# Kernel tuning notes

Hardware: AMD Instinct MI355X
Metric: run time of the kernel (lower is better)

Reference implementation:

```python
import jax, jax.numpy as jnp
import numpy as np

NOT_EPSILON = 1.0
B, Q, K, T = 2, 512, 512, 256  # batch, num queries, num keys, dims


def swishmax(x, axis):
    # x * exp(x - max) / (sum(|x * exp(x - max)|) + 1)
    xexp = x * jnp.exp(x - jnp.max(x, axis=axis, keepdims=True))
    return xexp / (jnp.sum(jnp.abs(xexp), axis=axis, keepdims=True) + NOT_EPSILON)


def setup_inputs() -> dict:
    key = jax.random.key(0)
    ks = jax.random.split(key, 8)
    s = 1.0 / np.sqrt(T)
    return {
        "query_tokens": jax.random.normal(ks[0], (B, Q, T), jnp.float32),
        "key_tokens": jax.random.normal(ks[1], (B, K, T), jnp.float32),
        "value_tokens": jax.random.normal(ks[2], (B, K, T), jnp.float32),
        "Wk": jax.random.normal(ks[3], (T, T), jnp.float32) * s,
        "Wq": jax.random.normal(ks[4], (T, T), jnp.float32) * s,
        "Wva": jax.random.normal(ks[5], (T, T), jnp.float32) * s,
        "Wal": jax.random.normal(ks[6], (T, T), jnp.float32) * s,
        "Wvo": jax.random.normal(ks[7], (T, T), jnp.float32) * s,
    }


def reference(query_tokens, key_tokens, value_tokens, Wk, Wq, Wva, Wal, Wvo):
    # torch nn.Linear: y = x @ W.T (no biases)
    k = jnp.einsum('bkt,ut->bku', key_tokens, Wk)      # [B,K,T]
    q = jnp.einsum('bqt,ut->bqu', query_tokens, Wq)    # [B,Q,T]
    # elementwise outer product over token pairs: [B,K,Q,T]
    raw = k[:, :, None, :] * q[:, None, :, :]
    logits = jnp.einsum('bkqt,ut->bkqu', raw, Wal)     # [B,K,Q,T]
    scale = swishmax(logits, axis=-2)                  # normalize over Q
    v = jnp.einsum('bkt,ut->bku', value_tokens, Wva)   # [B,K,T]
    values_scaled = v[:, :, None, :] * scale           # [B,K,Q,T]
    value_sum = values_scaled.sum(axis=-3)             # sum over K -> [B,Q,T]
    return jnp.einsum('bqt,ut->bqu', value_sum, Wvo)   # [B,Q,T]
```

## Files before the change

### kernel.cpp

```cpp
#include <hip/hip_runtime.h>
#include <cstdint>


typedef short bf16x8 __attribute__((ext_vector_type(8)));
typedef float f32x4  __attribute__((ext_vector_type(4)));

__device__ inline float bf2f(short s) {
  return __uint_as_float(((unsigned)(unsigned short)s) << 16);
}
__device__ inline unsigned packrn(float lo, float hi) {
  return __builtin_amdgcn_perm(__float_as_uint(hi) + 0x8000u,
                               __float_as_uint(lo) + 0x8000u, 0x07060302u);
}

#define FMA16()                                                                 \
  c[0][0] += a.x*w.x; c[0][1] += a.x*w.y; c[0][2] += a.x*w.z; c[0][3] += a.x*w.w; \
  c[1][0] += a.y*w.x; c[1][1] += a.y*w.y; c[1][2] += a.y*w.z; c[1][3] += a.y*w.w; \
  c[2][0] += a.z*w.x; c[2][1] += a.z*w.y; c[2][2] += a.z*w.z; c[2][3] += a.z*w.w; \
  c[3][0] += a.w*w.x; c[3][1] += a.w*w.y; c[3][2] += a.w*w.z; c[3][3] += a.w*w.w;

#define GEMM_BODY(X, WT)                                                        \
  __shared__ __align__(16) float As[16][68];                                    \
  __shared__ __align__(16) float Ws[16][64];                                    \
  const int tid = threadIdx.x;                                                  \
  const int tx4 = (tid & 15) * 4;                                               \
  const int ty4 = (tid >> 4) * 4;                                               \
  const int m0 = blockIdx.x * 64, u0 = blockIdx.y * 64;                         \
  const int lmi = tid >> 2, lc4 = (tid & 3) * 4;                                \
  const int lr  = tid >> 4, lu4 = (tid & 15) * 4;                               \
  float c[4][4] = {};                                                           \
  _Pragma("unroll 1")                                                           \
  for (int t0 = 0; t0 < 256; t0 += 16) {                                        \
    const float4 xa = *(const float4*)&(X)[(size_t)(m0 + lmi) * 256 + t0 + lc4];\
    const float4 wb = *(const float4*)&(WT)[(size_t)(t0 + lr) * 256 + u0 + lu4];\
    __syncthreads();                                                            \
    As[lc4 + 0][lmi] = xa.x; As[lc4 + 1][lmi] = xa.y;                           \
    As[lc4 + 2][lmi] = xa.z; As[lc4 + 3][lmi] = xa.w;                           \
    *(float4*)&Ws[lr][lu4] = wb;                                                \
    __syncthreads();                                                            \
    _Pragma("unroll")                                                           \
    for (int t = 0; t < 16; ++t) {                                              \
      const float4 a = *(const float4*)&As[t][ty4];                             \
      const float4 w = *(const float4*)&Ws[t][tx4];                             \
      FMA16();                                                                  \
    }                                                                           \
  }

__global__ __launch_bounds__(256) void prep(
    const float* __restrict__ Wk, const float* __restrict__ Wq,
    const float* __restrict__ Wva, const float* __restrict__ Wvo,
    const float* __restrict__ Wal, float* __restrict__ WT,
    short* __restrict__ WalF)
{
  const int r = blockIdx.x;
  const int m = blockIdx.y;
  const int t = threadIdx.x;
  if (m < 4) {
    const float* W = (m == 0) ? Wk : (m == 1) ? Wq : (m == 2) ? Wva : Wvo;
    WT[(size_t)m * 65536 + (size_t)t * 256 + r] = W[r * 256 + t];
  } else {
    const float v = Wal[r * 256 + t];
    const int uc = r >> 5, uu = r & 31, cc = t >> 3, j = t & 7;
    WalF[((size_t)(uc * 32 + cc) * 32 + uu) * 8 + j] = (short)packrn(v, v);
  }
}

__global__ __launch_bounds__(256) void proj3(
    const float* __restrict__ key, const float* __restrict__ value,
    const float* __restrict__ query, const float* __restrict__ WT,
    float* __restrict__ kproj, float* __restrict__ vproj, short* __restrict__ qpF)
{
  const int z = blockIdx.z;
  const float* X  = (z == 0) ? key : (z == 1) ? value : query;
  const float* Wt = WT + (size_t)((z == 0) ? 0 : (z == 1) ? 2 : 1) * 65536;
  GEMM_BODY(X, Wt);
  if (z == 2) {
    const int tbase = u0 + tx4;
    const int ks = tbase >> 5, l4f = (tbase & 31) >> 3, j0 = tbase & 7;
#pragma unroll
    for (int i = 0; i < 4; ++i) {
      const int m = m0 + ty4 + i;
      const int bb = m >> 9, q = m & 511;
      const int g = q >> 4, l15q = q & 15;
      const size_t idx = ((size_t)(((bb * 32 + g) * 8 + ks) * 64) + l4f * 16 + l15q) * 8 + j0;
      uint2 s; s.x = packrn(c[i][0], c[i][1]); s.y = packrn(c[i][2], c[i][3]);
      *(uint2*)&qpF[idx] = s;
    }
  } else {
    float* C = (z == 0) ? kproj : vproj;
#pragma unroll
    for (int i = 0; i < 4; ++i)
      *(float4*)&C[(size_t)(m0 + ty4 + i) * 256 + u0 + tx4] =
          make_float4(c[i][0], c[i][1], c[i][2], c[i][3]);
  }
}

__global__ __launch_bounds__(256) void gemm_out(
    const float* __restrict__ X, const float* __restrict__ WT, float* __restrict__ out)
{
  GEMM_BODY(X, WT);
#pragma unroll
  for (int i = 0; i < 4; ++i)
    *(float4*)&out[(size_t)(m0 + ty4 + i) * 256 + u0 + tx4] =
        make_float4(c[i][0], c[i][1], c[i][2], c[i][3]);
}

__global__ __launch_bounds__(1024, 4) void kernelC(
    const short* __restrict__ qpF, const float* __restrict__ kproj,
    const float* __restrict__ vproj, const short* __restrict__ WalF,
    float* __restrict__ vsum)
{
  __shared__ __align__(16) short W2F[8192];
  __shared__ float mS[16][32];
  __shared__ float sS[16][32];
  __shared__ float gS[32];

  const int kt = blockIdx.x, uc = blockIdx.y, b = blockIdx.z;
  const int u0 = uc * 32, k0 = kt * 32;
  const int tid = threadIdx.x;
  const int lane = tid & 63, w = tid >> 6;
  const int l15 = lane & 15, l4 = lane >> 4;
  const int c8 = tid >> 5;

  float wvf[8];
  {
    const bf16x8 wv = *(const bf16x8*)&WalF[((size_t)uc * 1024 + tid) * 8];
#pragma unroll
    for (int j = 0; j < 8; ++j) wvf[j] = bf2f(wv[j]);
  }

  const short* qbase = qpF + (size_t)b * 131072;
  const f32x4 z4 = {0.f, 0.f, 0.f, 0.f};
  f32x4 acc[2][2] = {z4, z4, z4, z4};

#pragma unroll 1
  for (int kk = 0; kk < 32; ++kk) {
    const int k = k0 + kk;
    const long krow = (long)(b * 512 + k) * 256;
    const f32x4 kp0 = *(const f32x4*)&kproj[krow + c8 * 8];
    const f32x4 kp1 = *(const f32x4*)&kproj[krow + c8 * 8 + 4];
    __syncthreads();
    {
      uint4 st;
      st.x = packrn(wvf[0] * kp0[0], wvf[1] * kp0[1]);
      st.y = packrn(wvf[2] * kp0[2], wvf[3] * kp0[3]);
      st.z = packrn(wvf[4] * kp1[0], wvf[5] * kp1[1]);
      st.w = packrn(wvf[6] * kp1[2], wvf[7] * kp1[3]);
      *(uint4*)&W2F[tid * 8] = st;
    }
    __syncthreads();

    f32x4 lg[2][2] = {z4, z4, z4, z4};
#pragma unroll
    for (int ks = 0; ks < 8; ++ks) {
      const bf16x8 qa0 = *(const bf16x8*)&qbase[(((w * 2 + 0) * 8 + ks) * 64 + lane) * 8];
      const bf16x8 qa1 = *(const bf16x8*)&qbase[(((w * 2 + 1) * 8 + ks) * 64 + lane) * 8];
      const bf16x8 wf0 = *(const bf16x8*)&W2F[(((ks * 4 + l4) * 32) + l15) * 8];
      const bf16x8 wf1 = *(const bf16x8*)&W2F[(((ks * 4 + l4) * 32) + 16 + l15) * 8];
      lg[0][0] = __builtin_amdgcn_mfma_f32_16x16x32_bf16(qa0, wf0, lg[0][0], 0, 0, 0);
      lg[1][0] = __builtin_amdgcn_mfma_f32_16x16x32_bf16(qa1, wf0, lg[1][0], 0, 0, 0);
      lg[0][1] = __builtin_amdgcn_mfma_f32_16x16x32_bf16(qa0, wf1, lg[0][1], 0, 0, 0);
      lg[1][1] = __builtin_amdgcn_mfma_f32_16x16x32_bf16(qa1, wf1, lg[1][1], 0, 0, 0);
    }

#pragma unroll
    for (int ug = 0; ug < 2; ++ug) {
      float m = lg[0][ug][0];
#pragma unroll
      for (int qg = 0; qg < 2; ++qg)
#pragma unroll
        for (int i = 0; i < 4; ++i) m = fmaxf(m, lg[qg][ug][i]);
      float s = 0.f;
#pragma unroll
      for (int qg = 0; qg < 2; ++qg)
#pragma unroll
        for (int i = 0; i < 4; ++i) {
          const float x = lg[qg][ug][i];
          const float p = x * __expf(x);
          lg[qg][ug][i] = p;
          s += fabsf(p);
        }
      m = fmaxf(m, __shfl_xor(m, 16));
      m = fmaxf(m, __shfl_xor(m, 32));
      s += __shfl_xor(s, 16);
      s += __shfl_xor(s, 32);
      if (l4 == 0) { mS[w][ug * 16 + l15] = m; sS[w][ug * 16 + l15] = s; }
    }
    __syncthreads();
    if (tid < 32) {
      float M = mS[0][tid], S = sS[0][tid];
#pragma unroll
      for (int r = 1; r < 16; ++r) { M = fmaxf(M, mS[r][tid]); S += sS[r][tid]; }
      const float em = __expf(-M);
      gS[tid] = vproj[krow + u0 + tid] * em / fmaf(S, em, 1.0f);
    }
    __syncthreads();
    const float g0 = gS[l15], g1 = gS[16 + l15];
#pragma unroll
    for (int qg = 0; qg < 2; ++qg)
#pragma unroll
      for (int i = 0; i < 4; ++i) {
        acc[qg][0][i] = fmaf(g0, lg[qg][0][i], acc[qg][0][i]);
        acc[qg][1][i] = fmaf(g1, lg[qg][1][i], acc[qg][1][i]);
      }
  }

#pragma unroll
  for (int qg = 0; qg < 2; ++qg)
#pragma unroll
    for (int ug = 0; ug < 2; ++ug)
#pragma unroll
      for (int i = 0; i < 4; ++i)
        atomicAdd(&vsum[(size_t)(b * 512 + w * 32 + qg * 16 + l4 * 4 + i) * 256 +
                        u0 + ug * 16 + l15],
                  acc[qg][ug][i]);
}

extern "C" void kernel_launch(void* const* d_in, const int* in_sizes, int n_in,
                              void* d_out, int out_size, void* d_ws, size_t ws_size,
                              hipStream_t stream) {
  const float* query = (const float*)d_in[0];
  const float* key   = (const float*)d_in[1];
  const float* value = (const float*)d_in[2];
  const float* Wk    = (const float*)d_in[3];
  const float* Wq    = (const float*)d_in[4];
  const float* Wva   = (const float*)d_in[5];
  const float* Wal   = (const float*)d_in[6];
  const float* Wvo   = (const float*)d_in[7];
  float* ws = (float*)d_ws;

  float* WT    = ws;
  float* kproj = ws + 262144;
  float* vproj = kproj + 262144;
  float* vsum  = vproj + 262144;
  short* qpF   = (short*)(vsum + 262144);
  short* WalF  = qpF + 262144;
  float* out   = (float*)d_out;

  hipMemsetAsync(vsum, 0, 262144 * sizeof(float), stream);

  prep<<<dim3(256, 5), 256, 0, stream>>>(Wk, Wq, Wva, Wvo, Wal, WT, WalF);
  proj3<<<dim3(16, 4, 3), 256, 0, stream>>>(key, value, query, WT, kproj, vproj, qpF);
  kernelC<<<dim3(16, 8, 2), 1024, 0, stream>>>(qpF, kproj, vproj, WalF, vsum);
  gemm_out<<<dim3(16, 4), 256, 0, stream>>>(vsum, WT + 3 * 65536, out);
}
```

Baseline: 211.6 us.

## Hoist query fragments into registers, stage vproj in LDS, fold memset into prep

The 16 bf16x8 query MFMA operands per wave are loaded into registers once, before the k loop, instead of being re-read from global memory on every one of the 32 iterations. The block's 32x32 vproj tile is staged in padded shared memory, and the reduction scratch arrays are padded to avoid bank conflicts. The vsum zeroing moves from a separate hipMemsetAsync into an extra grid row of the prep kernel. Launch bounds change from (1024,4) to (1024,1), giving the compiler the register budget the hoisted fragments need at the cost of fewer resident waves.

New measurement: 201.5 us. -4.8%, faster.

```diff
diff --git a/kernel.cpp b/kernel.cpp
--- a/kernel.cpp
+++ b/kernel.cpp
@@ -50,7 +50,7 @@
     const float* __restrict__ Wk, const float* __restrict__ Wq,
     const float* __restrict__ Wva, const float* __restrict__ Wvo,
     const float* __restrict__ Wal, float* __restrict__ WT,
-    short* __restrict__ WalF)
+    short* __restrict__ WalF, float* __restrict__ vsum)
 {
   const int r = blockIdx.x;
   const int m = blockIdx.y;
@@ -58,10 +58,12 @@
   if (m < 4) {
     const float* W = (m == 0) ? Wk : (m == 1) ? Wq : (m == 2) ? Wva : Wvo;
     WT[(size_t)m * 65536 + (size_t)t * 256 + r] = W[r * 256 + t];
-  } else {
+  } else if (m == 4) {
     const float v = Wal[r * 256 + t];
     const int uc = r >> 5, uu = r & 31, cc = t >> 3, j = t & 7;
     WalF[((size_t)(uc * 32 + cc) * 32 + uu) * 8 + j] = (short)packrn(v, v);
+  } else {
+    *(float4*)&vsum[(size_t)(r * 256 + t) * 4] = make_float4(0.f, 0.f, 0.f, 0.f);
   }
 }
 
@@ -105,14 +107,15 @@
         make_float4(c[i][0], c[i][1], c[i][2], c[i][3]);
 }
 
-__global__ __launch_bounds__(1024, 4) void kernelC(
+__global__ __launch_bounds__(1024, 1) void kernelC(
     const short* __restrict__ qpF, const float* __restrict__ kproj,
     const float* __restrict__ vproj, const short* __restrict__ WalF,
     float* __restrict__ vsum)
 {
   __shared__ __align__(16) short W2F[8192];
-  __shared__ float mS[16][32];
-  __shared__ float sS[16][32];
+  __shared__ float vpS[32 * 33];
+  __shared__ float mS[16 * 33];
+  __shared__ float sS[16 * 33];
   __shared__ float gS[32];
 
   const int kt = blockIdx.x, uc = blockIdx.y, b = blockIdx.z;
@@ -122,21 +125,28 @@
   const int l15 = lane & 15, l4 = lane >> 4;
   const int c8 = tid >> 5;
 
+  const bf16x8 wvb = *(const bf16x8*)&WalF[((size_t)uc * 1024 + tid) * 8];
   float wvf[8];
-  {
-    const bf16x8 wv = *(const bf16x8*)&WalF[((size_t)uc * 1024 + tid) * 8];
-#pragma unroll
-    for (int j = 0; j < 8; ++j) wvf[j] = bf2f(wv[j]);
-  }
+#pragma unroll
+  for (int j = 0; j < 8; ++j) wvf[j] = bf2f(wvb[j]);
+
+  vpS[(tid >> 5) * 33 + (tid & 31)] =
+      vproj[(size_t)(b * 512 + k0 + (tid >> 5)) * 256 + u0 + (tid & 31)];
 
   const short* qbase = qpF + (size_t)b * 131072;
+  bf16x8 qa[2][8];
+#pragma unroll
+  for (int qg = 0; qg < 2; ++qg)
+#pragma unroll
+    for (int ks = 0; ks < 8; ++ks)
+      qa[qg][ks] = *(const bf16x8*)&qbase[(((w * 2 + qg) * 8 + ks) * 64 + lane) * 8];
+
   const f32x4 z4 = {0.f, 0.f, 0.f, 0.f};
   f32x4 acc[2][2] = {z4, z4, z4, z4};
 
 #pragma unroll 1
   for (int kk = 0; kk < 32; ++kk) {
-    const int k = k0 + kk;
-    const long krow = (long)(b * 512 + k) * 256;
+    const long krow = (long)(b * 512 + k0 + kk) * 256;
     const f32x4 kp0 = *(const f32x4*)&kproj[krow + c8 * 8];
     const f32x4 kp1 = *(const f32x4*)&kproj[krow + c8 * 8 + 4];
     __syncthreads();
@@ -153,14 +163,12 @@
     f32x4 lg[2][2] = {z4, z4, z4, z4};
 #pragma unroll
     for (int ks = 0; ks < 8; ++ks) {
-      const bf16x8 qa0 = *(const bf16x8*)&qbase[(((w * 2 + 0) * 8 + ks) * 64 + lane) * 8];
-      const bf16x8 qa1 = *(const bf16x8*)&qbase[(((w * 2 + 1) * 8 + ks) * 64 + lane) * 8];
       const bf16x8 wf0 = *(const bf16x8*)&W2F[(((ks * 4 + l4) * 32) + l15) * 8];
       const bf16x8 wf1 = *(const bf16x8*)&W2F[(((ks * 4 + l4) * 32) + 16 + l15) * 8];
-      lg[0][0] = __builtin_amdgcn_mfma_f32_16x16x32_bf16(qa0, wf0, lg[0][0], 0, 0, 0);
-      lg[1][0] = __builtin_amdgcn_mfma_f32_16x16x32_bf16(qa1, wf0, lg[1][0], 0, 0, 0);
-      lg[0][1] = __builtin_amdgcn_mfma_f32_16x16x32_bf16(qa0, wf1, lg[0][1], 0, 0, 0);
-      lg[1][1] = __builtin_amdgcn_mfma_f32_16x16x32_bf16(qa1, wf1, lg[1][1], 0, 0, 0);
+      lg[0][0] = __builtin_amdgcn_mfma_f32_16x16x32_bf16(qa[0][ks], wf0, lg[0][0], 0, 0, 0);
+      lg[1][0] = __builtin_amdgcn_mfma_f32_16x16x32_bf16(qa[1][ks], wf0, lg[1][0], 0, 0, 0);
+      lg[0][1] = __builtin_amdgcn_mfma_f32_16x16x32_bf16(qa[0][ks], wf1, lg[0][1], 0, 0, 0);
+      lg[1][1] = __builtin_amdgcn_mfma_f32_16x16x32_bf16(qa[1][ks], wf1, lg[1][1], 0, 0, 0);
     }
 
 #pragma unroll
@@ -184,15 +192,15 @@
       m = fmaxf(m, __shfl_xor(m, 32));
       s += __shfl_xor(s, 16);
       s += __shfl_xor(s, 32);
-      if (l4 == 0) { mS[w][ug * 16 + l15] = m; sS[w][ug * 16 + l15] = s; }
+      if (l4 == 0) { mS[w * 33 + ug * 16 + l15] = m; sS[w * 33 + ug * 16 + l15] = s; }
     }
     __syncthreads();
     if (tid < 32) {
-      float M = mS[0][tid], S = sS[0][tid];
-#pragma unroll
-      for (int r = 1; r < 16; ++r) { M = fmaxf(M, mS[r][tid]); S += sS[r][tid]; }
+      float M = mS[tid], S = sS[tid];
+#pragma unroll
+      for (int r = 1; r < 16; ++r) { M = fmaxf(M, mS[r * 33 + tid]); S += sS[r * 33 + tid]; }
       const float em = __expf(-M);
-      gS[tid] = vproj[krow + u0 + tid] * em / fmaf(S, em, 1.0f);
+      gS[tid] = vpS[kk * 33 + tid] * em / fmaf(S, em, 1.0f);
     }
     __syncthreads();
     const float g0 = gS[l15], g1 = gS[16 + l15];
@@ -237,9 +245,7 @@
   short* WalF  = qpF + 262144;
   float* out   = (float*)d_out;
 
-  hipMemsetAsync(vsum, 0, 262144 * sizeof(float), stream);
-
-  prep<<<dim3(256, 5), 256, 0, stream>>>(Wk, Wq, Wva, Wvo, Wal, WT, WalF);
+  prep<<<dim3(256, 6), 256, 0, stream>>>(Wk, Wq, Wva, Wvo, Wal, WT, WalF, vsum);
   proj3<<<dim3(16, 4, 3), 256, 0, stream>>>(key, value, query, WT, kproj, vproj, qpF);
   kernelC<<<dim3(16, 8, 2), 1024, 0, stream>>>(qpF, kproj, vproj, WalF, vsum);
   gemm_out<<<dim3(16, 4), 256, 0, stream>>>(vsum, WT + 3 * 65536, out);
```
